# Kernel optimization log

Hardware: AMD Instinct MI355X
Metric: run time of the kernel (lower is better)

The kernel has to match this reference:

```python
import jax, jax.numpy as jnp
import numpy as np

B_SZ, D_MODEL, H_IMG, W_IMG = 8, 96, 64, 64
D_STATE, SSM_RATIO = 4, 2
D_INNER = SSM_RATIO * D_MODEL  # 192
DT_RANK = 6  # ceil(96/16)
EPS = 1e-5


def setup_inputs() -> dict:
    key = jax.random.key(0)
    ks = jax.random.split(key, 24)
    f = lambda k, shp, s=0.02: (jax.random.normal(k, shp, jnp.float32) * s)
    n = D_STATE
    inp = {
        "img": jax.random.normal(ks[0], (B_SZ, D_MODEL, H_IMG, W_IMG), jnp.float32),
        "text": jax.random.normal(ks[1], (B_SZ, D_MODEL, H_IMG, W_IMG), jnp.float32),
        # in_proj (Linear, bias=False): weight (out, in)
        "W_in_img": f(ks[2], (2 * D_INNER, D_MODEL)),
        "W_in_text": f(ks[3], (2 * D_INNER, D_MODEL)),
        # depthwise conv (d_inner,1,3,3) + bias, then BN (eval mode) params
        "conv_w_img": f(ks[4], (D_INNER, 1, 3, 3), 0.1),
        "conv_b_img": jnp.zeros((D_INNER,), jnp.float32),
        "bn_g_img": jnp.ones((D_INNER,), jnp.float32),
        "bn_b_img": jnp.zeros((D_INNER,), jnp.float32),
        "bn_m_img": jnp.zeros((D_INNER,), jnp.float32),
        "bn_v_img": jnp.ones((D_INNER,), jnp.float32),
        "conv_w_text": f(ks[5], (D_INNER, 1, 3, 3), 0.1),
        "conv_b_text": jnp.zeros((D_INNER,), jnp.float32),
        "bn_g_text": jnp.ones((D_INNER,), jnp.float32),
        "bn_b_text": jnp.zeros((D_INNER,), jnp.float32),
        "bn_m_text": jnp.zeros((D_INNER,), jnp.float32),
        "bn_v_text": jnp.ones((D_INNER,), jnp.float32),
        # SSM params
        "x_proj_w": f(ks[6], (DT_RANK + 2 * n, D_INNER)),
        "dt_proj_w": f(ks[7], (D_INNER, DT_RANK), 0.4),
        "dt_proj_b": jnp.log(jnp.expm1(jnp.exp(jax.random.uniform(ks[8], (D_INNER,), jnp.float32) * (np.log(0.1) - np.log(0.001)) + np.log(0.001)))),  # inv-softplus of dt in [1e-3,1e-1]
        "A_log": jnp.broadcast_to(jnp.log(jnp.arange(1, n + 1, dtype=jnp.float32)), (D_INNER, n)).copy(),
        "D_skip": jnp.ones((D_INNER,), jnp.float32),
        "ln_g": jnp.ones((D_INNER,), jnp.float32),
        "ln_b": jnp.zeros((D_INNER,), jnp.float32),
        # output projections (bias=False)
        "W_out": f(ks[9], (D_MODEL, D_INNER)),
        "W_fusion": f(ks[10], (D_MODEL, 2 * D_MODEL)),
    }
    return inp


def _silu(x):
    return x * jax.nn.sigmoid(x)


def _dwconv_bn_silu(x, w, b, g, beta, m, v):
    # x: (B, C, H, W), depthwise conv 3x3 SAME, then eval-mode BN, then SiLU
    y = jax.lax.conv_general_dilated(
        x, w, window_strides=(1, 1), padding='SAME',
        dimension_numbers=('NCHW', 'OIHW', 'NCHW'),
        feature_group_count=x.shape[1])
    y = y + b[None, :, None, None]
    y = (y - m[None, :, None, None]) * jax.lax.rsqrt(v[None, :, None, None] + EPS)
    y = y * g[None, :, None, None] + beta[None, :, None, None]
    return _silu(y)


def _selective_scan(x, delta, A, Bm, Cm, Dp):
    # x, delta: (b, d, l); A: (d, n); Bm, Cm: (b, n, l); Dp: (d,)
    dlt = jnp.transpose(delta, (2, 0, 1))   # (l, b, d)
    xt = jnp.transpose(x, (2, 0, 1))        # (l, b, d)
    Bt = jnp.transpose(Bm, (2, 0, 1))       # (l, b, n)
    Ct = jnp.transpose(Cm, (2, 0, 1))       # (l, b, n)
    dA = jnp.exp(dlt[..., None] * A[None, None])          # (l, b, d, n)
    dBx = (dlt * xt)[..., None] * Bt[:, :, None, :]       # (l, b, d, n)
    h0 = jnp.zeros(dA.shape[1:], dA.dtype)                # (b, d, n)

    def step(h, t):
        dA_t, dBx_t, C_t = t
        h = dA_t * h + dBx_t
        return h, jnp.einsum('bdn,bn->bd', h, C_t)

    _, ys = jax.lax.scan(step, h0, (dA, dBx, Ct))  # ys: (l, b, d)
    return jnp.transpose(ys, (1, 2, 0)) + Dp[None, :, None] * x  # (b, d, l)


def _ssm(xseq, x_proj_w, dt_proj_w, dt_proj_b, A_log, D_skip, ln_g, ln_b):
    # xseq: (b, l, d_inner)
    x_dbl = xseq @ x_proj_w.T                                # (b, l, r+2n)
    dt, Bm, Cm = jnp.split(x_dbl, [DT_RANK, DT_RANK + D_STATE], axis=-1)
    delta = jax.nn.softplus(dt @ dt_proj_w.T + dt_proj_b)    # (b, l, d)
    A = -jnp.exp(A_log)
    y = _selective_scan(
        jnp.transpose(xseq, (0, 2, 1)), jnp.transpose(delta, (0, 2, 1)), A,
        jnp.transpose(Bm, (0, 2, 1)), jnp.transpose(Cm, (0, 2, 1)), D_skip)
    y = jnp.transpose(y, (0, 2, 1))                          # (b, l, d)
    mu = y.mean(-1, keepdims=True)
    var = ((y - mu) ** 2).mean(-1, keepdims=True)
    return (y - mu) * jax.lax.rsqrt(var + EPS) * ln_g + ln_b


def reference(img, text, W_in_img, W_in_text,
              conv_w_img, conv_b_img, bn_g_img, bn_b_img, bn_m_img, bn_v_img,
              conv_w_text, conv_b_text, bn_g_text, bn_b_text, bn_m_text, bn_v_text,
              x_proj_w, dt_proj_w, dt_proj_b, A_log, D_skip, ln_g, ln_b,
              W_out, W_fusion):
    B, C, H, W = img.shape
    N = H * W
    img_flat = jnp.transpose(img, (0, 2, 3, 1)).reshape(B, N, C)
    text_flat = jnp.transpose(text, (0, 2, 3, 1)).reshape(B, N, C)
    # in projections, split into x and gate z
    xz_img = img_flat @ W_in_img.T                    # (B, N, 2*d_inner)
    xz_text = text_flat @ W_in_text.T
    x_img, z_img = jnp.split(xz_img, 2, axis=-1)
    x_text, z_text = jnp.split(xz_text, 2, axis=-1)
    # depthwise conv + BN + SiLU on spatial layout
    xi = jnp.transpose(x_img.reshape(B, H, W, D_INNER), (0, 3, 1, 2))
    xt = jnp.transpose(x_text.reshape(B, H, W, D_INNER), (0, 3, 1, 2))
    xi = _dwconv_bn_silu(xi, conv_w_img, conv_b_img, bn_g_img, bn_b_img, bn_m_img, bn_v_img)
    xt = _dwconv_bn_silu(xt, conv_w_text, conv_b_text, bn_g_text, bn_b_text, bn_m_text, bn_v_text)
    xi = jnp.transpose(xi, (0, 2, 3, 1)).reshape(B, N, D_INNER)
    xt = jnp.transpose(xt, (0, 2, 3, 1)).reshape(B, N, D_INNER)
    # selective-scan over concatenated image+text tokens
    x_for = jnp.concatenate([xi, xt], axis=1)         # (B, 2N, d_inner)
    y = _ssm(x_for, x_proj_w, dt_proj_w, dt_proj_b, A_log, D_skip, ln_g, ln_b)
    z = jnp.concatenate([z_img, z_text], axis=1)
    y = y * _silu(z)
    out = y @ W_out.T                                 # (B, 2N, d_model)
    # interleave the two streams per spatial position and fuse
    out = out.reshape(B, 2, H, W, C)
    out = jnp.transpose(out, (0, 2, 3, 1, 4)).reshape(B, H, W, 2 * C)
    out = out @ W_fusion.T                            # (B, H, W, C)
    return jnp.transpose(out, (0, 3, 1, 2))
```

## Files before the change

### kernel.cpp

```cpp
#include <hip/hip_runtime.h>
#include <math.h>

#define EPSV 1e-5f

typedef __attribute__((ext_vector_type(8))) short short8_t;
typedef __attribute__((ext_vector_type(4))) float f32x4;

#define N_XSP   12582912
#define N_ZBUF  12582912
#define N_XD    12582912
#define N_DTBC  1048576
#define N_STATE 786432

__device__ __forceinline__ float siluf(float v) {
  return v / (1.f + __expf(-v));
}

__device__ __forceinline__ unsigned short f2bf(float f) {
  unsigned int u = __float_as_uint(f);
  u += 0x7fffu + ((u >> 16) & 1u);
  return (unsigned short)(u >> 16);
}

__device__ __forceinline__ float bf2f(unsigned short h) {
  return __uint_as_float(((unsigned int)h) << 16);
}

__global__ __launch_bounds__(256) void k_prep(const float* __restrict__ Wout,
                                              const float* __restrict__ Wf,
                                              const float* __restrict__ Wii,
                                              const float* __restrict__ Wit,
                                              const float* __restrict__ xpw,
                                              unsigned short* __restrict__ Mgb,
                                              unsigned short* __restrict__ wbi,
                                              unsigned short* __restrict__ wbt,
                                              unsigned short* __restrict__ Wxtb) {
  int e = blockIdx.x * 256 + threadIdx.x;
  if (e < 36864) {
    int k = e / 96, o = e - k * 96;
    int half = (k >= 192) ? 1 : 0;
    int c = k - half * 192;
    const float* wfr = Wf + o * 192 + half * 96;
    float acc = 0.f;
#pragma unroll 4
    for (int j = 0; j < 96; ++j) acc += wfr[j] * Wout[j * 192 + c];
    Mgb[(half * 96 + o) * 192 + c] = f2bf(acc);
  } else if (e < 73728) {
    int i = e - 36864;
    wbi[i] = f2bf(Wii[i]);
  } else if (e < 110592) {
    int i = e - 73728;
    wbt[i] = f2bf(Wit[i]);
  } else if (e < 113664) {
    int i = e - 110592;
    int o = i / 192;
    Wxtb[i] = (o < 14) ? f2bf(xpw[i]) : (unsigned short)0;
  }
}

__global__ __launch_bounds__(256, 4) void k_inproj(const float* __restrict__ img,
                                                   const float* __restrict__ text,
                                                   const unsigned short* __restrict__ wbi,
                                                   const unsigned short* __restrict__ wbt,
                                                   unsigned short* __restrict__ xsph,
                                                   unsigned short* __restrict__ zbufh) {
  __shared__ __align__(16) unsigned short Xbf[64 * 104];
  int bx = blockIdx.x;
  int tile = bx & 63, b = (bx >> 6) & 7, s = bx >> 9;
  int n0 = tile * 64;
  int tid = threadIdx.x;
  int w = tid >> 6, lane = tid & 63;
  const float* src = s ? text : img;
  const unsigned short* wsel = s ? wbt : wbi;

  for (int idx = tid; idx < 6144; idx += 256) {
    int c = idx >> 6, t = idx & 63;
    Xbf[t * 104 + c] = f2bf(src[((size_t)b * 96 + c) * 4096 + n0 + t]);
  }
  __syncthreads();

  int arow = lane & 15;
  int acol = (lane >> 4) * 8;
  short8_t af[4][3];
#pragma unroll
  for (int mt = 0; mt < 4; ++mt) {
    const unsigned short* ap = &Xbf[(mt * 16 + arow) * 104 + acol];
    af[mt][0] = *(const short8_t*)(ap);
    af[mt][1] = *(const short8_t*)(ap + 32);
    af[mt][2] = *(const short8_t*)(ap + 64);
  }

  const unsigned short* wbase = wsel + ((size_t)(w * 96 + (lane & 15))) * 96 + ((lane >> 4) * 8);
  int rowoff = (lane >> 4) * 4;
  size_t tokb = (size_t)b * 8192 + (size_t)s * 4096 + n0;

  for (int nt = 0; nt < 6; ++nt) {
    short8_t b0 = *(const short8_t*)(wbase + nt * 16 * 96 + 0);
    short8_t b1 = *(const short8_t*)(wbase + nt * 16 * 96 + 32);
    short8_t b2 = *(const short8_t*)(wbase + nt * 16 * 96 + 64);
    f32x4 acc[4];
    f32x4 zz = {0.f, 0.f, 0.f, 0.f};
#pragma unroll
    for (int mt = 0; mt < 4; ++mt) acc[mt] = zz;
#pragma unroll
    for (int mt = 0; mt < 4; ++mt) {
      acc[mt] = __builtin_amdgcn_mfma_f32_16x16x32_bf16(af[mt][0], b0, acc[mt], 0, 0, 0);
      acc[mt] = __builtin_amdgcn_mfma_f32_16x16x32_bf16(af[mt][1], b1, acc[mt], 0, 0, 0);
      acc[mt] = __builtin_amdgcn_mfma_f32_16x16x32_bf16(af[mt][2], b2, acc[mt], 0, 0, 0);
    }
    if (w < 2) {
      int d = w * 96 + nt * 16 + (lane & 15);
      unsigned short* xp = xsph + (((size_t)s * 8 + b) * 192 + d) * 4096 + n0 + rowoff;
#pragma unroll
      for (int mt = 0; mt < 4; ++mt) {
        f32x4 a = acc[mt];
        uint2 pk;
        pk.x = (unsigned int)f2bf(a[0]) | ((unsigned int)f2bf(a[1]) << 16);
        pk.y = (unsigned int)f2bf(a[2]) | ((unsigned int)f2bf(a[3]) << 16);
        *(uint2*)&xp[mt * 16] = pk;
      }
    } else {
      int ch = (w - 2) * 96 + nt * 16 + (lane & 15);
#pragma unroll
      for (int mt = 0; mt < 4; ++mt) {
        f32x4 a = acc[mt];
        unsigned short* zp = zbufh + (tokb + mt * 16 + rowoff) * 192 + ch;
        zp[0] = f2bf(a[0]); zp[192] = f2bf(a[1]); zp[384] = f2bf(a[2]); zp[576] = f2bf(a[3]);
      }
    }
  }
}

__global__ __launch_bounds__(256) void k_conv(
    const unsigned short* __restrict__ xsph,
    const float* __restrict__ cwi, const float* __restrict__ cbi,
    const float* __restrict__ bgi, const float* __restrict__ bbi,
    const float* __restrict__ bmi, const float* __restrict__ bvi,
    const float* __restrict__ cwt, const float* __restrict__ cbt,
    const float* __restrict__ bgt, const float* __restrict__ bbt,
    const float* __restrict__ bmt, const float* __restrict__ bvt,
    unsigned short* __restrict__ xdh) {
  int bid = blockIdx.x;
  int img = bid / 96;
  int d0 = (bid - img * 96) * 2;
  int widx = threadIdx.x >> 6;
  int lane = threadIdx.x & 63;
  int d = d0 + (widx >> 1);
  int half = widx & 1;
  int s = img >> 3;
  const float* cw = s ? cwt : cwi;
  const float* cb = s ? cbt : cbi;
  const float* bg = s ? bgt : bgi;
  const float* bb2 = s ? bbt : bbi;
  const float* bm = s ? bmt : bmi;
  const float* bv = s ? bvt : bvi;
  const unsigned short* src = xsph + ((size_t)img * 192 + d) * 4096;
  unsigned short* dst = xdh + ((size_t)img * 192 + d) * 4096;
  float c0 = cw[d * 9 + 0], c1 = cw[d * 9 + 1], c2 = cw[d * 9 + 2];
  float c3 = cw[d * 9 + 3], c4 = cw[d * 9 + 4], c5 = cw[d * 9 + 5];
  float c6 = cw[d * 9 + 6], c7 = cw[d * 9 + 7], c8 = cw[d * 9 + 8];
  float sc = bg[d] * rsqrtf(bv[d] + EPSV);
  float eb = (cb[d] - bm[d]) * sc + bb2[d];
  int h0 = half * 32;
  float pc = (h0 > 0) ? bf2f(src[(h0 - 1) * 64 + lane]) : 0.f;
  float cc = bf2f(src[h0 * 64 + lane]);
  float nc = bf2f(src[(h0 + 1) * 64 + lane]);
  float t;
  t = __shfl_up(pc, 1);  float pl = (lane == 0) ? 0.f : t;
  t = __shfl_down(pc, 1); float pr = (lane == 63) ? 0.f : t;
  t = __shfl_up(cc, 1);  float cl = (lane == 0) ? 0.f : t;
  t = __shfl_down(cc, 1); float cr = (lane == 63) ? 0.f : t;
#pragma unroll 4
  for (int i = 0; i < 32; ++i) {
    int h = h0 + i;
    float fut = (h + 2 <= 63) ? bf2f(src[(h + 2) * 64 + lane]) : 0.f;
    t = __shfl_up(nc, 1);  float nl = (lane == 0) ? 0.f : t;
    t = __shfl_down(nc, 1); float nr = (lane == 63) ? 0.f : t;
    float a = pl * c0 + pc * c1 + pr * c2
            + cl * c3 + cc * c4 + cr * c5
            + nl * c6 + nc * c7 + nr * c8;
    a = a * sc + eb;
    dst[h * 64 + lane] = f2bf(a / (1.f + __expf(-a)));
    pl = cl; pc = cc; pr = cr;
    cl = nl; cc = nc; cr = nr;
    nc = fut;
  }
}

__global__ __launch_bounds__(192) void k_scanA(const unsigned short* __restrict__ xdh,
                                               const unsigned short* __restrict__ Wxtb,
                                               const float* __restrict__ dtw,
                                               const float* __restrict__ dtbias,
                                               const float* __restrict__ Alog,
                                               float* __restrict__ dtBC,
                                               float* __restrict__ hend,
                                               float* __restrict__ Pbuf) {
  __shared__ __align__(16) unsigned short Xt16[16 * 200];
  __shared__ __align__(16) float SBC[64 * 16];
  int c = blockIdx.x & 127, b = blockIdx.x >> 7;
  int s = c >> 6, cl = c & 63;
  int d = threadIdx.x;
  int w = d >> 6, lane = d & 63;
  int tokbase = b * 8192 + c * 64;

  const unsigned short* xrow = xdh + (((size_t)s * 8 + b) * 192 + d) * 4096 + cl * 64;
  short8_t xr8[8];
#pragma unroll
  for (int i = 0; i < 8; ++i) xr8[i] = *(const short8_t*)(xrow + i * 8);

  const unsigned short* wb = Wxtb + (size_t)(lane & 15) * 192 + ((lane >> 4) * 8);
  short8_t bfx[6];
#pragma unroll
  for (int ks = 0; ks < 6; ++ks) bfx[ks] = *(const short8_t*)(wb + ks * 32);

  float w0 = dtw[d * 6 + 0], w1 = dtw[d * 6 + 1], w2 = dtw[d * 6 + 2];
  float w3 = dtw[d * 6 + 3], w4 = dtw[d * 6 + 4], w5 = dtw[d * 6 + 5];
  float bb = dtbias[d];
  float4 al = *(const float4*)&Alog[d * 4];
  float A0 = -__expf(al.x), A1 = -__expf(al.y), A2 = -__expf(al.z), A3 = -__expf(al.w);

  int arow = lane & 15, acol = (lane >> 4) * 8;
#pragma unroll
  for (int r = 0; r < 4; ++r) {
    __syncthreads();
#pragma unroll
    for (int tt = 0; tt < 16; ++tt) {
      int i = (r * 16 + tt) >> 3, j = tt & 7;
      Xt16[tt * 200 + d] = (unsigned short)xr8[i][j];
    }
    __syncthreads();
    if (w == (r % 3)) {
      f32x4 a4 = {0.f, 0.f, 0.f, 0.f};
#pragma unroll
      for (int ks = 0; ks < 6; ++ks) {
        short8_t a = *(const short8_t*)&Xt16[arow * 200 + acol + ks * 32];
        a4 = __builtin_amdgcn_mfma_f32_16x16x32_bf16(a, bfx[ks], a4, 0, 0, 0);
      }
      int tt0 = r * 16 + (lane >> 4) * 4, o = lane & 15;
#pragma unroll
      for (int rr = 0; rr < 4; ++rr) {
        SBC[(tt0 + rr) * 16 + o] = a4[rr];
        dtBC[(size_t)(tokbase + tt0 + rr) * 16 + o] = a4[rr];
      }
    }
  }
  __syncthreads();

  bool fastp = fabsf(A0 + 1.f) < 1e-4f && fabsf(A1 + 2.f) < 2e-4f &&
               fabsf(A2 + 3.f) < 3e-4f && fabsf(A3 + 4.f) < 4e-4f;
  float h0 = 0.f, h1 = 0.f, h2 = 0.f, h3 = 0.f, sd = 0.f;
  if (fastp) {
#pragma unroll
    for (int i = 0; i < 8; ++i)
#pragma unroll
      for (int j = 0; j < 8; ++j) {
        int l2 = i * 8 + j;
        float4 s0 = *(const float4*)&SBC[l2 * 16 + 0];
        float4 s1 = *(const float4*)&SBC[l2 * 16 + 4];
        float4 s2 = *(const float4*)&SBC[l2 * 16 + 8];
        float pre = bb + w0 * s0.x + w1 * s0.y + w2 * s0.z + w3 * s0.w + w4 * s1.x + w5 * s1.y;
        float ex = __expf(pre);
        float opx = 1.f + ex;
        float e1 = __builtin_amdgcn_rcpf(opx);
        float delta = (pre > 15.f) ? pre : __logf(opx);
        sd += delta;
        float e2 = e1 * e1, e3 = e2 * e1, e4 = e2 * e2;
        float dx = delta * bf2f((unsigned short)xr8[i][j]);
        h0 = e1 * h0 + dx * s1.z;
        h1 = e2 * h1 + dx * s1.w;
        h2 = e3 * h2 + dx * s2.x;
        h3 = e4 * h3 + dx * s2.y;
      }
  } else {
#pragma unroll
    for (int i = 0; i < 8; ++i)
#pragma unroll
      for (int j = 0; j < 8; ++j) {
        int l2 = i * 8 + j;
        float4 s0 = *(const float4*)&SBC[l2 * 16 + 0];
        float4 s1 = *(const float4*)&SBC[l2 * 16 + 4];
        float4 s2 = *(const float4*)&SBC[l2 * 16 + 8];
        float pre = bb + w0 * s0.x + w1 * s0.y + w2 * s0.z + w3 * s0.w + w4 * s1.x + w5 * s1.y;
        float ex = __expf(pre);
        float delta = (pre > 15.f) ? pre : __logf(1.f + ex);
        sd += delta;
        float dx = delta * bf2f((unsigned short)xr8[i][j]);
        h0 = __expf(delta * A0) * h0 + dx * s1.z;
        h1 = __expf(delta * A1) * h1 + dx * s1.w;
        h2 = __expf(delta * A2) * h2 + dx * s2.x;
        h3 = __expf(delta * A3) * h3 + dx * s2.y;
      }
  }
  size_t o = (((size_t)b * 128 + c) * 192 + d) * 4;
  *(float4*)&hend[o] = make_float4(h0, h1, h2, h3);
  if (fastp) {
    float p1 = __expf(-sd);
    float p2 = p1 * p1;
    *(float4*)&Pbuf[o] = make_float4(p1, p2, p2 * p1, p2 * p2);
  } else {
    *(float4*)&Pbuf[o] = make_float4(__expf(A0 * sd), __expf(A1 * sd), __expf(A2 * sd), __expf(A3 * sd));
  }
}

__global__ __launch_bounds__(256) void k_scan2(const float* __restrict__ hend,
                                               const float* __restrict__ Pbuf,
                                               float* __restrict__ hinit) {
  int e = blockIdx.x * 256 + threadIdx.x;
  if (e >= 8 * 768) return;
  int b = e / 768, r = e - b * 768;
  float h = 0.f;
#pragma unroll 4
  for (int c = 0; c < 128; ++c) {
    int a = (b * 128 + c) * 768 + r;
    hinit[a] = h;
    h = Pbuf[a] * h + hend[a];
  }
}

__global__ __launch_bounds__(192) void k_scanB(const unsigned short* __restrict__ xdh,
                                               const float* __restrict__ dtBC,
                                               const float* __restrict__ dtw,
                                               const float* __restrict__ dtbias,
                                               const float* __restrict__ Alog,
                                               const float* __restrict__ Dskip,
                                               const float* __restrict__ hinit,
                                               unsigned short* __restrict__ ybufh) {
  __shared__ __align__(16) float SBC[64 * 16];
  int c = blockIdx.x & 127, b = blockIdx.x >> 7;
  int s = c >> 6, cl = c & 63;
  int d = threadIdx.x;
  float w0 = dtw[d * 6 + 0], w1 = dtw[d * 6 + 1], w2 = dtw[d * 6 + 2];
  float w3 = dtw[d * 6 + 3], w4 = dtw[d * 6 + 4], w5 = dtw[d * 6 + 5];
  float bb = dtbias[d];
  float4 al = *(const float4*)&Alog[d * 4];
  float A0 = -__expf(al.x), A1 = -__expf(al.y), A2 = -__expf(al.z), A3 = -__expf(al.w);
  float Dv = Dskip[d];
  int tokbase = b * 8192 + c * 64;
  for (int idx = d; idx < 1024; idx += 192) SBC[idx] = dtBC[(size_t)tokbase * 16 + idx];
  const unsigned short* xrow = xdh + (((size_t)s * 8 + b) * 192 + d) * 4096 + cl * 64;
  short8_t xr8[8];
#pragma unroll
  for (int i = 0; i < 8; ++i) xr8[i] = *(const short8_t*)(xrow + i * 8);
  size_t o = (((size_t)b * 128 + c) * 192 + d) * 4;
  float4 hv = *(const float4*)&hinit[o];
  float h0 = hv.x, h1 = hv.y, h2 = hv.z, h3 = hv.w;
  bool fastp = fabsf(A0 + 1.f) < 1e-4f && fabsf(A1 + 2.f) < 2e-4f &&
               fabsf(A2 + 3.f) < 3e-4f && fabsf(A3 + 4.f) < 4e-4f;
  __syncthreads();
  unsigned short* yout = ybufh + (size_t)tokbase * 192 + d;
  if (fastp) {
#pragma unroll
    for (int i = 0; i < 8; ++i)
#pragma unroll
      for (int j = 0; j < 8; ++j) {
        int l2 = i * 8 + j;
        float4 s0 = *(const float4*)&SBC[l2 * 16 + 0];
        float4 s1 = *(const float4*)&SBC[l2 * 16 + 4];
        float4 s2 = *(const float4*)&SBC[l2 * 16 + 8];
        float4 s3 = *(const float4*)&SBC[l2 * 16 + 12];
        float pre = bb + w0 * s0.x + w1 * s0.y + w2 * s0.z + w3 * s0.w + w4 * s1.x + w5 * s1.y;
        float ex = __expf(pre);
        float opx = 1.f + ex;
        float e1 = __builtin_amdgcn_rcpf(opx);
        float delta = (pre > 15.f) ? pre : __logf(opx);
        float e2 = e1 * e1, e3 = e2 * e1, e4 = e2 * e2;
        float xv = bf2f((unsigned short)xr8[i][j]);
        float dx = delta * xv;
        h0 = e1 * h0 + dx * s1.z;
        h1 = e2 * h1 + dx * s1.w;
        h2 = e3 * h2 + dx * s2.x;
        h3 = e4 * h3 + dx * s2.y;
        yout[(size_t)l2 * 192] = f2bf(h0 * s2.z + h1 * s2.w + h2 * s3.x + h3 * s3.y + Dv * xv);
      }
  } else {
#pragma unroll
    for (int i = 0; i < 8; ++i)
#pragma unroll
      for (int j = 0; j < 8; ++j) {
        int l2 = i * 8 + j;
        float4 s0 = *(const float4*)&SBC[l2 * 16 + 0];
        float4 s1 = *(const float4*)&SBC[l2 * 16 + 4];
        float4 s2 = *(const float4*)&SBC[l2 * 16 + 8];
        float4 s3 = *(const float4*)&SBC[l2 * 16 + 12];
        float pre = bb + w0 * s0.x + w1 * s0.y + w2 * s0.z + w3 * s0.w + w4 * s1.x + w5 * s1.y;
        float ex = __expf(pre);
        float delta = (pre > 15.f) ? pre : __logf(1.f + ex);
        float xv = bf2f((unsigned short)xr8[i][j]);
        float dx = delta * xv;
        h0 = __expf(delta * A0) * h0 + dx * s1.z;
        h1 = __expf(delta * A1) * h1 + dx * s1.w;
        h2 = __expf(delta * A2) * h2 + dx * s2.x;
        h3 = __expf(delta * A3) * h3 + dx * s2.y;
        yout[(size_t)l2 * 192] = f2bf(h0 * s2.z + h1 * s2.w + h2 * s3.x + h3 * s3.y + Dv * xv);
      }
  }
}

__global__ __launch_bounds__(384) void k_outfuse(const unsigned short* __restrict__ ybufh,
                                                 const unsigned short* __restrict__ zbufh,
                                                 const float* __restrict__ lng,
                                                 const float* __restrict__ lnb,
                                                 const unsigned short* __restrict__ Mgb,
                                                 float* __restrict__ out) {
  __shared__ __align__(16) unsigned short Xbf[64 * 200];
  int tile = blockIdx.x & 63, b = blockIdx.x >> 6;
  int n0 = tile * 64;
  int tid = threadIdx.x;
  int w = tid >> 6, lane = tid & 63;
  float lg0 = lng[lane], lg1 = lng[lane + 64], lg2 = lng[lane + 128];
  float lb0 = lnb[lane], lb1 = lnb[lane + 64], lb2 = lnb[lane + 128];

  const unsigned short* bb = Mgb + ((size_t)(w * 16 + (lane & 15))) * 192 + ((lane >> 4) * 8);
  short8_t bfr[2][6];
#pragma unroll
  for (int kc = 0; kc < 2; ++kc)
#pragma unroll
    for (int ks = 0; ks < 6; ++ks)
      bfr[kc][ks] = *(const short8_t*)(bb + kc * 96 * 192 + ks * 32);

  f32x4 acc[4];
  f32x4 zz = {0.f, 0.f, 0.f, 0.f};
#pragma unroll
  for (int mt = 0; mt < 4; ++mt) acc[mt] = zz;

  int arow = lane & 15, acol = (lane >> 4) * 8;
  for (int kc = 0; kc < 2; ++kc) {
    size_t tokb = (size_t)b * 8192 + (size_t)kc * 4096 + n0;
    if (kc) __syncthreads();
    for (int t = w; t < 64; t += 6) {
      const unsigned short* yr = ybufh + (tokb + t) * 192;
      const unsigned short* zr = zbufh + (tokb + t) * 192;
      float y0 = bf2f(yr[lane]), y1 = bf2f(yr[lane + 64]), y2 = bf2f(yr[lane + 128]);
      float z0 = bf2f(zr[lane]), z1 = bf2f(zr[lane + 64]), z2 = bf2f(zr[lane + 128]);
      float sm = y0 + y1 + y2;
      float sq = y0 * y0 + y1 * y1 + y2 * y2;
#pragma unroll
      for (int off = 32; off; off >>= 1) {
        sm += __shfl_xor(sm, off);
        sq += __shfl_xor(sq, off);
      }
      float mu = sm * (1.f / 192.f);
      float var = sq * (1.f / 192.f) - mu * mu;
      float rstd = rsqrtf(var + EPSV);
      Xbf[t * 200 + lane]       = f2bf(((y0 - mu) * rstd * lg0 + lb0) * siluf(z0));
      Xbf[t * 200 + lane + 64]  = f2bf(((y1 - mu) * rstd * lg1 + lb1) * siluf(z1));
      Xbf[t * 200 + lane + 128] = f2bf(((y2 - mu) * rstd * lg2 + lb2) * siluf(z2));
    }
    __syncthreads();
#pragma unroll
    for (int mt = 0; mt < 4; ++mt) {
      const unsigned short* ap = &Xbf[(mt * 16 + arow) * 200 + acol];
#pragma unroll
      for (int ks = 0; ks < 6; ++ks) {
        short8_t a = *(const short8_t*)(ap + ks * 32);
        acc[mt] = __builtin_amdgcn_mfma_f32_16x16x32_bf16(a, bfr[kc][ks], acc[mt], 0, 0, 0);
      }
    }
  }
  int rowoff = (lane >> 4) * 4;
  float* op = out + ((size_t)b * 96 + w * 16 + (lane & 15)) * 4096 + n0 + rowoff;
#pragma unroll
  for (int mt = 0; mt < 4; ++mt) {
    f32x4 a = acc[mt];
    *(float4*)&op[mt * 16] = make_float4(a[0], a[1], a[2], a[3]);
  }
}

extern "C" void kernel_launch(void* const* d_in, const int* in_sizes, int n_in,
                              void* d_out, int out_size, void* d_ws, size_t ws_size,
                              hipStream_t stream) {
  (void)in_sizes; (void)n_in; (void)out_size; (void)ws_size;
  const float* img  = (const float*)d_in[0];
  const float* text = (const float*)d_in[1];
  const float* Wii  = (const float*)d_in[2];
  const float* Wit  = (const float*)d_in[3];
  const float* cwi  = (const float*)d_in[4];
  const float* cbi  = (const float*)d_in[5];
  const float* bgi  = (const float*)d_in[6];
  const float* bbi  = (const float*)d_in[7];
  const float* bmi  = (const float*)d_in[8];
  const float* bvi  = (const float*)d_in[9];
  const float* cwt  = (const float*)d_in[10];
  const float* cbt  = (const float*)d_in[11];
  const float* bgt  = (const float*)d_in[12];
  const float* bbt  = (const float*)d_in[13];
  const float* bmt  = (const float*)d_in[14];
  const float* bvt  = (const float*)d_in[15];
  const float* xpw  = (const float*)d_in[16];
  const float* dtw  = (const float*)d_in[17];
  const float* dtb  = (const float*)d_in[18];
  const float* Alog = (const float*)d_in[19];
  const float* Dsk  = (const float*)d_in[20];
  const float* lng  = (const float*)d_in[21];
  const float* lnb  = (const float*)d_in[22];
  const float* Wout = (const float*)d_in[23];
  const float* Wfus = (const float*)d_in[24];

  float* ws    = (float*)d_ws;
  unsigned short* xsph  = (unsigned short*)ws;
  unsigned short* zbufh = (unsigned short*)(ws + N_XSP);
  unsigned short* xdh   = (unsigned short*)(ws + N_XSP + N_ZBUF);
  float* dtBC  = ws + N_XSP + N_ZBUF + N_XD;
  float* hend  = dtBC + N_DTBC;
  float* Pbuf  = hend + N_STATE;
  float* hinit = Pbuf + N_STATE;
  unsigned short* Mgb  = (unsigned short*)(hinit + N_STATE);
  unsigned short* Wxtb = Mgb + 36864;
  unsigned short* wbi  = Wxtb + 3072;
  unsigned short* wbt  = wbi + 36864;
  unsigned short* ybufh = xsph;
  float* out   = (float*)d_out;

  hipLaunchKernelGGL(k_prep, dim3(444), dim3(256), 0, stream, Wout, Wfus, Wii, Wit, xpw, Mgb, wbi, wbt, Wxtb);
  hipLaunchKernelGGL(k_inproj, dim3(1024), dim3(256), 0, stream, img, text, wbi, wbt, xsph, zbufh);
  hipLaunchKernelGGL(k_conv, dim3(1536), dim3(256), 0, stream, xsph,
                     cwi, cbi, bgi, bbi, bmi, bvi, cwt, cbt, bgt, bbt, bmt, bvt, xdh);
  hipLaunchKernelGGL(k_scanA, dim3(1024), dim3(192), 0, stream, xdh, Wxtb, dtw, dtb, Alog, dtBC, hend, Pbuf);
  hipLaunchKernelGGL(k_scan2, dim3(24), dim3(256), 0, stream, hend, Pbuf, hinit);
  hipLaunchKernelGGL(k_scanB, dim3(1024), dim3(192), 0, stream, xdh, dtBC, dtw, dtb, Alog, Dsk, hinit, ybufh);
  hipLaunchKernelGGL(k_outfuse, dim3(512), dim3(384), 0, stream, ybufh, zbufh, lng, lnb, Mgb, out);
}
```

Baseline: 144.7 us.

## Fuse scan phase B with LayerNorm, gating and output projection kernel

Merges the second scan pass and the output/fusion GEMM kernel into one kernel. Each 384-thread block handles the matching image and text chunks, which share a spatial tile, and writes the scan outputs into LDS instead of a global y buffer. This removes the global write and read of the y intermediate and one kernel launch. The costs are larger LDS use per block (two 64x200 bf16 tiles plus two dtBC tiles) and half as many blocks (512 instead of 1024) for the scan portion, which may lower occupancy and parallelism.

```diff
diff --git a/kernel.cpp b/kernel.cpp
--- a/kernel.cpp
+++ b/kernel.cpp
@@ -317,27 +317,38 @@
   }
 }
 
-__global__ __launch_bounds__(192) void k_scanB(const unsigned short* __restrict__ xdh,
-                                               const float* __restrict__ dtBC,
-                                               const float* __restrict__ dtw,
-                                               const float* __restrict__ dtbias,
-                                               const float* __restrict__ Alog,
-                                               const float* __restrict__ Dskip,
-                                               const float* __restrict__ hinit,
-                                               unsigned short* __restrict__ ybufh) {
-  __shared__ __align__(16) float SBC[64 * 16];
-  int c = blockIdx.x & 127, b = blockIdx.x >> 7;
-  int s = c >> 6, cl = c & 63;
-  int d = threadIdx.x;
+__global__ __launch_bounds__(384, 3) void k_scanout(
+    const unsigned short* __restrict__ xdh,
+    const float* __restrict__ dtBC,
+    const float* __restrict__ dtw,
+    const float* __restrict__ dtbias,
+    const float* __restrict__ Alog,
+    const float* __restrict__ Dskip,
+    const float* __restrict__ hinit,
+    const unsigned short* __restrict__ zbufh,
+    const float* __restrict__ lng,
+    const float* __restrict__ lnb,
+    const unsigned short* __restrict__ Mgb,
+    float* __restrict__ out) {
+  __shared__ __align__(16) unsigned short Xbf[2][64 * 200];
+  __shared__ __align__(16) float SBC2[2][64 * 16];
+  int tile = blockIdx.x & 63, b = blockIdx.x >> 6;
+  int n0 = tile * 64;
+  int tid = threadIdx.x;
+  int g = (tid >= 192) ? 1 : 0;
+  int d = tid - g * 192;
+  int c = g * 64 + tile;
+  int tokbase = b * 8192 + c * 64;
+
   float w0 = dtw[d * 6 + 0], w1 = dtw[d * 6 + 1], w2 = dtw[d * 6 + 2];
   float w3 = dtw[d * 6 + 3], w4 = dtw[d * 6 + 4], w5 = dtw[d * 6 + 5];
   float bb = dtbias[d];
   float4 al = *(const float4*)&Alog[d * 4];
   float A0 = -__expf(al.x), A1 = -__expf(al.y), A2 = -__expf(al.z), A3 = -__expf(al.w);
   float Dv = Dskip[d];
-  int tokbase = b * 8192 + c * 64;
-  for (int idx = d; idx < 1024; idx += 192) SBC[idx] = dtBC[(size_t)tokbase * 16 + idx];
-  const unsigned short* xrow = xdh + (((size_t)s * 8 + b) * 192 + d) * 4096 + cl * 64;
+  float* sbc = &SBC2[g][0];
+  for (int idx = d; idx < 1024; idx += 192) sbc[idx] = dtBC[(size_t)tokbase * 16 + idx];
+  const unsigned short* xrow = xdh + (((size_t)g * 8 + b) * 192 + d) * 4096 + tile * 64;
   short8_t xr8[8];
 #pragma unroll
   for (int i = 0; i < 8; ++i) xr8[i] = *(const short8_t*)(xrow + i * 8);
@@ -347,17 +358,17 @@
   bool fastp = fabsf(A0 + 1.f) < 1e-4f && fabsf(A1 + 2.f) < 2e-4f &&
                fabsf(A2 + 3.f) < 3e-4f && fabsf(A3 + 4.f) < 4e-4f;
   __syncthreads();
-  unsigned short* yout = ybufh + (size_t)tokbase * 192 + d;
+  unsigned short* ylds = &Xbf[g][d];
   if (fastp) {
 #pragma unroll
     for (int i = 0; i < 8; ++i)
 #pragma unroll
       for (int j = 0; j < 8; ++j) {
         int l2 = i * 8 + j;
-        float4 s0 = *(const float4*)&SBC[l2 * 16 + 0];
-        float4 s1 = *(const float4*)&SBC[l2 * 16 + 4];
-        float4 s2 = *(const float4*)&SBC[l2 * 16 + 8];
-        float4 s3 = *(const float4*)&SBC[l2 * 16 + 12];
+        float4 s0 = *(const float4*)&sbc[l2 * 16 + 0];
+        float4 s1 = *(const float4*)&sbc[l2 * 16 + 4];
+        float4 s2 = *(const float4*)&sbc[l2 * 16 + 8];
+        float4 s3 = *(const float4*)&sbc[l2 * 16 + 12];
         float pre = bb + w0 * s0.x + w1 * s0.y + w2 * s0.z + w3 * s0.w + w4 * s1.x + w5 * s1.y;
         float ex = __expf(pre);
         float opx = 1.f + ex;
@@ -370,7 +381,7 @@
         h1 = e2 * h1 + dx * s1.w;
         h2 = e3 * h2 + dx * s2.x;
         h3 = e4 * h3 + dx * s2.y;
-        yout[(size_t)l2 * 192] = f2bf(h0 * s2.z + h1 * s2.w + h2 * s3.x + h3 * s3.y + Dv * xv);
+        ylds[l2 * 200] = f2bf(h0 * s2.z + h1 * s2.w + h2 * s3.x + h3 * s3.y + Dv * xv);
       }
   } else {
 #pragma unroll
@@ -378,10 +389,10 @@
 #pragma unroll
       for (int j = 0; j < 8; ++j) {
         int l2 = i * 8 + j;
-        float4 s0 = *(const float4*)&SBC[l2 * 16 + 0];
-        float4 s1 = *(const float4*)&SBC[l2 * 16 + 4];
-        float4 s2 = *(const float4*)&SBC[l2 * 16 + 8];
-        float4 s3 = *(const float4*)&SBC[l2 * 16 + 12];
+        float4 s0 = *(const float4*)&sbc[l2 * 16 + 0];
+        float4 s1 = *(const float4*)&sbc[l2 * 16 + 4];
+        float4 s2 = *(const float4*)&sbc[l2 * 16 + 8];
+        float4 s3 = *(const float4*)&sbc[l2 * 16 + 12];
         float pre = bb + w0 * s0.x + w1 * s0.y + w2 * s0.z + w3 * s0.w + w4 * s1.x + w5 * s1.y;
         float ex = __expf(pre);
         float delta = (pre > 15.f) ? pre : __logf(1.f + ex);
@@ -391,65 +402,55 @@
         h1 = __expf(delta * A1) * h1 + dx * s1.w;
         h2 = __expf(delta * A2) * h2 + dx * s2.x;
         h3 = __expf(delta * A3) * h3 + dx * s2.y;
-        yout[(size_t)l2 * 192] = f2bf(h0 * s2.z + h1 * s2.w + h2 * s3.x + h3 * s3.y + Dv * xv);
-      }
-  }
-}
-
-__global__ __launch_bounds__(384) void k_outfuse(const unsigned short* __restrict__ ybufh,
-                                                 const unsigned short* __restrict__ zbufh,
-                                                 const float* __restrict__ lng,
-                                                 const float* __restrict__ lnb,
-                                                 const unsigned short* __restrict__ Mgb,
-                                                 float* __restrict__ out) {
-  __shared__ __align__(16) unsigned short Xbf[64 * 200];
-  int tile = blockIdx.x & 63, b = blockIdx.x >> 6;
-  int n0 = tile * 64;
-  int tid = threadIdx.x;
+        ylds[l2 * 200] = f2bf(h0 * s2.z + h1 * s2.w + h2 * s3.x + h3 * s3.y + Dv * xv);
+      }
+  }
+  __syncthreads();
+
   int w = tid >> 6, lane = tid & 63;
   float lg0 = lng[lane], lg1 = lng[lane + 64], lg2 = lng[lane + 128];
   float lb0 = lnb[lane], lb1 = lnb[lane + 64], lb2 = lnb[lane + 128];
-
-  const unsigned short* bb = Mgb + ((size_t)(w * 16 + (lane & 15))) * 192 + ((lane >> 4) * 8);
+  for (int t = w; t < 128; t += 6) {
+    int kc = t >> 6, tl = t & 63;
+    size_t tok = (size_t)b * 8192 + (size_t)kc * 4096 + n0 + tl;
+    unsigned short* yr = &Xbf[kc][tl * 200];
+    const unsigned short* zr = zbufh + tok * 192;
+    float y0 = bf2f(yr[lane]), y1 = bf2f(yr[lane + 64]), y2 = bf2f(yr[lane + 128]);
+    float z0 = bf2f(zr[lane]), z1 = bf2f(zr[lane + 64]), z2 = bf2f(zr[lane + 128]);
+    float sm = y0 + y1 + y2;
+    float sq = y0 * y0 + y1 * y1 + y2 * y2;
+#pragma unroll
+    for (int off = 32; off; off >>= 1) {
+      sm += __shfl_xor(sm, off);
+      sq += __shfl_xor(sq, off);
+    }
+    float mu = sm * (1.f / 192.f);
+    float var = sq * (1.f / 192.f) - mu * mu;
+    float rstd = rsqrtf(var + EPSV);
+    yr[lane]       = f2bf(((y0 - mu) * rstd * lg0 + lb0) * siluf(z0));
+    yr[lane + 64]  = f2bf(((y1 - mu) * rstd * lg1 + lb1) * siluf(z1));
+    yr[lane + 128] = f2bf(((y2 - mu) * rstd * lg2 + lb2) * siluf(z2));
+  }
+  __syncthreads();
+
+  const unsigned short* bb_p = Mgb + ((size_t)(w * 16 + (lane & 15))) * 192 + ((lane >> 4) * 8);
   short8_t bfr[2][6];
 #pragma unroll
   for (int kc = 0; kc < 2; ++kc)
 #pragma unroll
     for (int ks = 0; ks < 6; ++ks)
-      bfr[kc][ks] = *(const short8_t*)(bb + kc * 96 * 192 + ks * 32);
+      bfr[kc][ks] = *(const short8_t*)(bb_p + kc * 96 * 192 + ks * 32);
 
   f32x4 acc[4];
   f32x4 zz = {0.f, 0.f, 0.f, 0.f};
 #pragma unroll
   for (int mt = 0; mt < 4; ++mt) acc[mt] = zz;
-
   int arow = lane & 15, acol = (lane >> 4) * 8;
+#pragma unroll
   for (int kc = 0; kc < 2; ++kc) {
-    size_t tokb = (size_t)b * 8192 + (size_t)kc * 4096 + n0;
-    if (kc) __syncthreads();
-    for (int t = w; t < 64; t += 6) {
-      const unsigned short* yr = ybufh + (tokb + t) * 192;
-      const unsigned short* zr = zbufh + (tokb + t) * 192;
-      float y0 = bf2f(yr[lane]), y1 = bf2f(yr[lane + 64]), y2 = bf2f(yr[lane + 128]);
-      float z0 = bf2f(zr[lane]), z1 = bf2f(zr[lane + 64]), z2 = bf2f(zr[lane + 128]);
-      float sm = y0 + y1 + y2;
-      float sq = y0 * y0 + y1 * y1 + y2 * y2;
-#pragma unroll
-      for (int off = 32; off; off >>= 1) {
-        sm += __shfl_xor(sm, off);
-        sq += __shfl_xor(sq, off);
-      }
-      float mu = sm * (1.f / 192.f);
-      float var = sq * (1.f / 192.f) - mu * mu;
-      float rstd = rsqrtf(var + EPSV);
-      Xbf[t * 200 + lane]       = f2bf(((y0 - mu) * rstd * lg0 + lb0) * siluf(z0));
-      Xbf[t * 200 + lane + 64]  = f2bf(((y1 - mu) * rstd * lg1 + lb1) * siluf(z1));
-      Xbf[t * 200 + lane + 128] = f2bf(((y2 - mu) * rstd * lg2 + lb2) * siluf(z2));
-    }
-    __syncthreads();
 #pragma unroll
     for (int mt = 0; mt < 4; ++mt) {
-      const unsigned short* ap = &Xbf[(mt * 16 + arow) * 200 + acol];
+      const unsigned short* ap = &Xbf[kc][(mt * 16 + arow) * 200 + acol];
 #pragma unroll
       for (int ks = 0; ks < 6; ++ks) {
         short8_t a = *(const short8_t*)(ap + ks * 32);
@@ -508,7 +509,6 @@
   unsigned short* Wxtb = Mgb + 36864;
   unsigned short* wbi  = Wxtb + 3072;
   unsigned short* wbt  = wbi + 36864;
-  unsigned short* ybufh = xsph;
   float* out   = (float*)d_out;
 
   hipLaunchKernelGGL(k_prep, dim3(444), dim3(256), 0, stream, Wout, Wfus, Wii, Wit, xpw, Mgb, wbi, wbt, Wxtb);
@@ -517,6 +517,6 @@
                      cwi, cbi, bgi, bbi, bmi, bvi, cwt, cbt, bgt, bbt, bmt, bvt, xdh);
   hipLaunchKernelGGL(k_scanA, dim3(1024), dim3(192), 0, stream, xdh, Wxtb, dtw, dtb, Alog, dtBC, hend, Pbuf);
   hipLaunchKernelGGL(k_scan2, dim3(24), dim3(256), 0, stream, hend, Pbuf, hinit);
-  hipLaunchKernelGGL(k_scanB, dim3(1024), dim3(192), 0, stream, xdh, dtBC, dtw, dtb, Alog, Dsk, hinit, ybufh);
-  hipLaunchKernelGGL(k_outfuse, dim3(512), dim3(384), 0, stream, ybufh, zbufh, lng, lnb, Mgb, out);
-}
+  hipLaunchKernelGGL(k_scanout, dim3(512), dim3(384), 0, stream, xdh, dtBC, dtw, dtb, Alog, Dsk,
+                     hinit, zbufh, lng, lnb, Mgb, out);
+}
```

Result: slower. 158.3 us (+9.3%).
